# Performance work log

Measured on AMD Instinct MI355X. Metric: run time of the kernel, lower is better.

Reference implementation:

```python
import jax, jax.numpy as jnp
import numpy as np

L = 8192            # sequence length
V = 100000          # vocab size
E = 256             # embedding dim
H = 512             # lstm hidden dim (bidirectional total)
HD = H // 2         # per-direction hidden
TAGS = 32
T = TAGS + 2        # tagset + START/STOP
START = T - 2       # START_TAG = -2
STOP = T - 1        # STOP_TAG = -1
NEG = -10000.0


def setup_inputs() -> dict:
    key = jax.random.key(0)
    ks = jax.random.split(key, 11)
    s = 0.05
    return {
        "input_words": jax.random.randint(ks[0], (L,), 0, V),
        "embed": jax.random.normal(ks[1], (V, E), dtype=jnp.float32) * s,
        "Wih_f": jax.random.normal(ks[2], (4 * HD, E), dtype=jnp.float32) * s,
        "Whh_f": jax.random.normal(ks[3], (4 * HD, HD), dtype=jnp.float32) * s,
        "b_f": jax.random.normal(ks[4], (4 * HD,), dtype=jnp.float32) * s,
        "Wih_b": jax.random.normal(ks[5], (4 * HD, E), dtype=jnp.float32) * s,
        "Whh_b": jax.random.normal(ks[6], (4 * HD, HD), dtype=jnp.float32) * s,
        "b_b": jax.random.normal(ks[7], (4 * HD,), dtype=jnp.float32) * s,
        "W_out": jax.random.normal(ks[8], (T, H), dtype=jnp.float32) * s,
        "b_out": jax.random.normal(ks[9], (T,), dtype=jnp.float32) * s,
        "transitions": jax.random.normal(ks[10], (T, T), dtype=jnp.float32),
    }


def _lstm_dir(x, Wih, Whh, b, reverse):
    # single-layer LSTM, one direction; torch gate order i, f, g, o
    def step(carry, xt):
        h, c = carry
        g = xt @ Wih.T + h @ Whh.T + b
        i, f, gg, o = jnp.split(g, 4)
        i = jax.nn.sigmoid(i)
        f = jax.nn.sigmoid(f)
        gg = jnp.tanh(gg)
        o = jax.nn.sigmoid(o)
        c = f * c + i * gg
        h = o * jnp.tanh(c)
        return (h, c), h

    init = (jnp.zeros((HD,), x.dtype), jnp.zeros((HD,), x.dtype))
    _, hs = jax.lax.scan(step, init, x, reverse=reverse)
    return hs  # (L, HD)


def _crf_marginals(feats, transitions):
    lse = jax.nn.logsumexp
    # forward algorithm: alpha_t[j] = lse_i(alpha_{t-1}[i] + trans[j,i]) + feat_t[j]
    def fstep(alpha, feat):
        new = lse(alpha[None, :] + transitions, axis=1) + feat
        return new, new

    alpha0 = jnp.full((T,), NEG, feats.dtype).at[START].set(0.0)
    alphaL, log_alpha = jax.lax.scan(fstep, alpha0, feats)  # (L, T)

    # backward algorithm, replicating repo's init: beta_L[j] = lse_i(trans[i, j])
    beta_last = lse(transitions, axis=0)

    # beta_t[j] = lse_i(beta_{t+1}[i] + feat_{t+1}[i] + trans[i, j])
    def bstep(beta, feat_next):
        new = lse((beta + feat_next)[:, None] + transitions, axis=0)
        return new, new

    _, betas = jax.lax.scan(bstep, beta_last, feats[1:], reverse=True)
    log_beta = jnp.concatenate([betas, beta_last[None]], axis=0)  # (L, T)
    return log_alpha + log_beta


def reference(input_words, embed, Wih_f, Whh_f, b_f, Wih_b, Whh_b, b_b,
              W_out, b_out, transitions):
    x = embed[input_words]                           # (L, E)
    hf = _lstm_dir(x, Wih_f, Whh_f, b_f, reverse=False)
    hb = _lstm_dir(x, Wih_b, Whh_b, b_b, reverse=True)
    lstm_out = jnp.concatenate([hf, hb], axis=-1)    # (L, H)
    feats = lstm_out @ W_out.T + b_out               # (L, T)
    score = _crf_marginals(feats, transitions)       # (L, T)
    tags = jnp.argmax(score, axis=1)                 # (L,)
    return score, tags
```

## Files before the change

### kernel.cpp

```cpp
#include <hip/hip_runtime.h>
#include <cstdint>
#include <cstddef>

#define LSEQ 8192
#define NT   34
#define NP   36
#define SCH  64
#define CCH  128
#define F_L2E 1.4426950408889634f
#define F_LN2 0.6931471805599453f

typedef int v4i __attribute__((ext_vector_type(4)));

#if __has_builtin(__builtin_amdgcn_global_load_lds)
#define HAS_GLL 1
#else
#define HAS_GLL 0
#endif

#if __has_builtin(__builtin_amdgcn_mfma_i32_16x16x64_i8)
#define MFMA_I8(a,b,c) __builtin_amdgcn_mfma_i32_16x16x64_i8((a),(b),(c),0,0,0)
#else
__device__ __forceinline__ v4i mfma_i8_asm(v4i a, v4i b, v4i c){
  asm volatile("v_mfma_i32_16x16x64_i8 %0, %1, %2, %0\n\ts_nop 7\n\ts_nop 7"
               : "+v"(c) : "v"(a), "v"(b));
  return c;
}
#define MFMA_I8(a,b,c) mfma_i8_asm((a),(b),(c))
#endif

__device__ __forceinline__ float ex2(float x){
#if __has_builtin(__builtin_amdgcn_exp2f)
  return __builtin_amdgcn_exp2f(x);
#else
  return exp2f(x);
#endif
}
__device__ __forceinline__ float lg2(float x){
#if __has_builtin(__builtin_amdgcn_logf)
  return __builtin_amdgcn_logf(x);
#else
  return __log2f(x);
#endif
}

__device__ __forceinline__ float sigf(float x){
  return __fdividef(1.f, 1.f + ex2(-F_L2E * x));
}
__device__ __forceinline__ float tanhf_fast(float x){
  return 1.f - __fdividef(2.f, ex2(2.f * F_L2E * x) + 1.f);
}

__device__ __forceinline__ void barrier_lds(){
  asm volatile("s_waitcnt lgkmcnt(0)\n\ts_barrier" ::: "memory");
}

__global__ void k_quant(const float* __restrict__ Whh_f,
                        const float* __restrict__ Whh_b,
                        int* __restrict__ Wq, float* __restrict__ fac){
  int bid = blockIdx.x;
  int dir = bid >> 10;
  int r   = bid & 1023;
  int i   = threadIdx.x;
  const float* W = (dir ? Whh_b : Whh_f) + r * 256 + i * 4;
  float w0 = W[0], w1 = W[1], w2 = W[2], w3 = W[3];
  float m = fmaxf(fmaxf(fabsf(w0), fabsf(w1)), fmaxf(fabsf(w2), fabsf(w3)));
  for (int s = 32; s; s >>= 1) m = fmaxf(m, __shfl_xor(m, s));
  float scale = (m > 0.f) ? m / 127.f : 1.f;
  float inv = __fdividef(1.f, scale);
  int q0 = (int)rintf(w0 * inv), q1 = (int)rintf(w1 * inv);
  int q2 = (int)rintf(w2 * inv), q3 = (int)rintf(w3 * inv);
  q0 = max(-127, min(127, q0)); q1 = max(-127, min(127, q1));
  q2 = max(-127, min(127, q2)); q3 = max(-127, min(127, q3));
  int p = (q0 & 255) | ((q1 & 255) << 8) | ((q2 & 255) << 16) | ((q3 & 255) << 24);
  Wq[(dir << 16) + (r << 6) + i] = p;
  if (i == 0) fac[(dir << 10) + r] = scale * (1.f / 127.f);
}

__global__ void k_gproj(const int* __restrict__ words,
                        const float* __restrict__ embed,
                        const float* __restrict__ Wih_f, const float* __restrict__ b_f,
                        const float* __restrict__ Wih_b, const float* __restrict__ b_b,
                        float* __restrict__ G_f, float* __restrict__ G_b){
  int dir = blockIdx.y;
  const float* Wih = dir ? Wih_b : Wih_f;
  const float* bb  = dir ? b_b  : b_f;
  float* G = dir ? G_b : G_f;
  int t0 = blockIdx.x * 16;
  __shared__ __align__(16) float X[16 * 256];
  for (int idx = threadIdx.x; idx < 16 * 256; idx += 256) {
    int tt = idx >> 8, e = idx & 255;
    X[idx] = embed[(size_t)words[t0 + tt] * 256 + e];
  }
  __syncthreads();
  const float4* X4 = (const float4*)X;
  for (int rb = 0; rb < 4; rb++) {
    int r = rb * 256 + threadIdx.x;
    float bv = bb[r];
    float acc[16];
#pragma unroll
    for (int tt = 0; tt < 16; tt++) acc[tt] = bv;
    const float4* W4 = (const float4*)(Wih + (size_t)r * 256);
    for (int eb = 0; eb < 64; eb++) {
      float4 w = W4[eb];
#pragma unroll
      for (int tt = 0; tt < 16; tt++) {
        float4 x = X4[tt * 64 + eb];
        acc[tt] += w.x * x.x + w.y * x.y + w.z * x.z + w.w * x.w;
      }
    }
    for (int tt = 0; tt < 16; tt++)
      G[(size_t)(t0 + tt) * 1024 + (threadIdx.x << 2) + rb] = acc[tt];
  }
}

__global__ __launch_bounds__(512, 2) void k_lstm(const int* __restrict__ Wq,
                                                 const float* __restrict__ fac,
                                                 const float* __restrict__ G_f,
                                                 const float* __restrict__ G_b,
                                                 float* __restrict__ hf,
                                                 float* __restrict__ hb){
  int dir = blockIdx.x;
  const int* Wqd = Wq + (dir << 16);
  const float* facp = fac + (dir << 10);
  const float* G = dir ? G_b : G_f;
  float* hout = dir ? hb : hf;
  int tid = threadIdx.x;
  int ln  = tid & 63;
  int wv  = tid >> 6;
  int lg  = ln >> 4;
  int lr  = ln & 15;
  int h_l = (lr >> 2) & 1;
  int r_l = lr & 3;
  int u   = (wv << 5) + (h_l << 4) + (lg << 2) + r_l;

  __shared__ __align__(16) float GL[2][4 * 1024];
  __shared__ __align__(16) int h8c[2][64];

  v4i wgt[4][2][4];
#pragma unroll
  for (int g = 0; g < 4; g++)
#pragma unroll
    for (int h = 0; h < 2; h++) {
      int R = g * 256 + (wv << 5) + (h << 4) + lr;
#pragma unroll
      for (int ks = 0; ks < 4; ks++)
        wgt[g][h][ks] = *(const v4i*)(Wqd + R * 64 + ks * 16 + lg * 4);
    }

  float fI = facp[u], fF = facp[u + 256], fG = facp[u + 512], fO = facp[u + 768];
  if (tid < 64) h8c[0][tid] = 0;
  float c = 0.f;
  v4i zero = {0, 0, 0, 0};

  auto stage = [&](int cn) {
    int half = cn & 1;
    int gt0 = dir ? (8191 - (cn * 4 + 3)) : (cn * 4);
    const char* src = (const char*)(G + (size_t)gt0 * 1024) + (wv << 11) + (ln << 4);
    char* dst = (char*)&GL[half][0] + (wv << 11);
#pragma unroll
    for (int i = 0; i < 2; i++) {
#if HAS_GLL
      __builtin_amdgcn_global_load_lds(
          (const __attribute__((address_space(1))) unsigned int*)(src + (i << 10)),
          (__attribute__((address_space(3))) unsigned int*)(dst + (i << 10)),
          16, 0, 0);
#else
      *(float4*)(dst + (i << 10) + (ln << 4)) = *(const float4*)(src + (i << 10));
#endif
    }
  };

  auto step = [&](int t, const float* Grow, const int* bufR, int* bufW) {
    const v4i* hb4 = (const v4i*)bufR;
    v4i b0 = hb4[lg], b1 = hb4[4 + lg], b2 = hb4[8 + lg], b3 = hb4[12 + lg];
    float4 gv = ((const float4*)Grow)[u];
    v4i res[4][2];
#pragma unroll
    for (int g = 0; g < 4; g++)
#pragma unroll
      for (int h = 0; h < 2; h++)
        res[g][h] = MFMA_I8(wgt[g][h][0], b0, zero);
#pragma unroll
    for (int g = 0; g < 4; g++)
#pragma unroll
      for (int h = 0; h < 2; h++)
        res[g][h] = MFMA_I8(wgt[g][h][1], b1, res[g][h]);
#pragma unroll
    for (int g = 0; g < 4; g++)
#pragma unroll
      for (int h = 0; h < 2; h++)
        res[g][h] = MFMA_I8(wgt[g][h][2], b2, res[g][h]);
#pragma unroll
    for (int g = 0; g < 4; g++)
#pragma unroll
      for (int h = 0; h < 2; h++)
        res[g][h] = MFMA_I8(wgt[g][h][3], b3, res[g][h]);
    bool sh = h_l != 0;
    bool s1 = (r_l & 1) != 0;
    bool s2 = (r_l & 2) != 0;
    v4i tI = sh ? res[0][1] : res[0][0];
    v4i tF = sh ? res[1][1] : res[1][0];
    v4i tG = sh ? res[2][1] : res[2][0];
    v4i tO = sh ? res[3][1] : res[3][0];
    int vI = s2 ? (s1 ? tI.w : tI.z) : (s1 ? tI.y : tI.x);
    int vF = s2 ? (s1 ? tF.w : tF.z) : (s1 ? tF.y : tF.x);
    int vG = s2 ? (s1 ? tG.w : tG.z) : (s1 ? tG.y : tG.x);
    int vO = s2 ? (s1 ? tO.w : tO.z) : (s1 ? tO.y : tO.x);
    float ri = (float)vI * fI + gv.x;
    float rf = (float)vF * fF + gv.y;
    float rg = (float)vG * fG + gv.z;
    float ro = (float)vO * fO + gv.w;
    float is = sigf(ri), fs = sigf(rf);
    float gt = tanhf_fast(rg), os = sigf(ro);
    c = fs * c + is * gt;
    float hv = os * tanhf_fast(c);
    int q = ((int)rintf(hv * 127.f)) & 255;
    int x = q << (r_l * 8);
#if __has_builtin(__builtin_amdgcn_mov_dpp)
    x += __builtin_amdgcn_mov_dpp(x, 0xB1, 0xF, 0xF, true);
    x += __builtin_amdgcn_mov_dpp(x, 0x4E, 0xF, 0xF, true);
#else
    x += __shfl_xor(x, 1);
    x += __shfl_xor(x, 2);
#endif
    if (r_l == 0 && lr < 8) bufW[u >> 2] = x;
    if (lr < 8) {
      int time = dir ? (8191 - t) : t;
      hout[(size_t)time * 256 + u] = hv;
    }
  };

  stage(0);
  asm volatile("s_waitcnt vmcnt(0)" ::: "memory");
  __syncthreads();

  int cur = 0;
  for (int cn = 0; cn < 2048; ++cn) {
    if (cn + 1 < 2048) stage(cn + 1);
    const float* Hc = GL[cn & 1];
#pragma unroll
    for (int s = 0; s < 4; ++s) {
      int row = dir ? (3 - s) : s;
      step((cn << 2) + s, Hc + (row << 10), h8c[cur], h8c[cur ^ 1]);
      cur ^= 1;
      if (s == 3) {
        asm volatile("s_waitcnt vmcnt(0) lgkmcnt(0)\n\ts_barrier" ::: "memory");
      } else {
        barrier_lds();
      }
    }
  }
}

__global__ void k_feats(const float* __restrict__ hf, const float* __restrict__ hb,
                        const float* __restrict__ W_out, const float* __restrict__ b_out,
                        float* __restrict__ feats){
  int t0 = blockIdx.x * 16;
  for (int oi = threadIdx.x; oi < 16 * NT; oi += 256) {
    int tt = oi / NT;
    int tag = oi - tt * NT;
    int t = t0 + tt;
    const float4* w4 = (const float4*)(W_out + (size_t)tag * 512);
    const float4* a4 = (const float4*)(hf + (size_t)t * 256);
    const float4* c4 = (const float4*)(hb + (size_t)t * 256);
    float acc = b_out[tag];
    for (int k = 0; k < 64; k++) {
      float4 w = w4[k]; float4 h = a4[k];
      acc += w.x * h.x + w.y * h.y + w.z * h.z + w.w * h.w;
    }
    for (int k = 0; k < 64; k++) {
      float4 w = w4[64 + k]; float4 h = c4[k];
      acc += w.x * h.x + w.y * h.y + w.z * h.z + w.w * h.w;
    }
    feats[(size_t)t * NT + tag] = acc;
  }
}

__global__ __launch_bounds__(320) void k_crf_p1(const float* __restrict__ feats,
                                                const float* __restrict__ trans,
                                                float* __restrict__ Pg,
                                                float* __restrict__ rmaxG){
  int dir = blockIdx.x >> 7;
  int c   = blockIdx.x & (CCH - 1);
  int tid = threadIdx.x;
  int t0  = c * SCH;

  __shared__ __align__(16) float TRM[NT * NP];
  __shared__ float Fe[(SCH + 1) * NT];
  __shared__ __align__(16) float Pbuf[2][NT * NP];
  __shared__ float CM[NP];
  __shared__ float RMs[NT];

  for (int idx = tid; idx < NT * NT; idx += 320) {
    int j = idx / NT, k = idx - j * NT;
    float v = (dir == 0) ? trans[j * NT + k] : trans[k * NT + j];
    TRM[j * NP + k] = v * F_L2E;
  }
  for (int idx = tid; idx < (SCH + 1) * NT; idx += 320) {
    int s = idx / NT, j = idx - s * NT;
    int t = t0 + s; if (t > LSEQ - 1) t = LSEQ - 1;
    Fe[idx] = feats[(size_t)t * NT + j] * F_L2E;
  }
  for (int idx = tid; idx < NT * NP; idx += 320) {
    int k = idx / NP, i = idx - k * NP;
    Pbuf[0][idx] = (i < NT && i == k) ? 0.f : -1e30f;
  }
  if (tid < NP) CM[tid] = (tid < NT) ? 0.f : -1e30f;
  __syncthreads();
  if (tid < NT) {
    float m = -3e38f;
    for (int k = 0; k < NT; k++) m = fmaxf(m, TRM[tid * NP + k]);
    RMs[tid] = m;
  }
  __syncthreads();
  for (int idx = tid; idx < NT * NT; idx += 320) {
    int j = idx / NT, k = idx - j * NT;
    TRM[j * NP + k] -= RMs[j];
  }
  __syncthreads();

  int cur = 0;
  int j = tid / 9, g = tid - (tid / 9) * 9;
  bool act = (tid < 306);
  int i0 = 4 * g;

  for (int s = 0; s < SCH; s++) {
    int t = (dir == 0) ? (t0 + s) : (t0 + SCH - 1 - s);
    if (dir == 1 && t == LSEQ - 1) continue;
    const float* Pc = Pbuf[cur];
    float* Pn = Pbuf[cur ^ 1];
    if (act) {
      float cm0 = CM[i0], cm1 = CM[i0 + 1], cm2 = CM[i0 + 2], cm3 = CM[i0 + 3];
      float s0 = 0, s1 = 0, s2 = 0, s3 = 0;
      const float* trp = TRM + j * NP;
      const float* fep = Fe + (t + 1 - t0) * NT;
#pragma unroll
      for (int k = 0; k < NT; k++) {
        float trv = trp[k];
        if (dir == 1) trv += fep[k];
        float4 p = *(const float4*)&Pc[k * NP + i0];
        s0 += ex2(trv + p.x - cm0);
        s1 += ex2(trv + p.y - cm1);
        s2 += ex2(trv + p.z - cm2);
        s3 += ex2(trv + p.w - cm3);
      }
      float base = RMs[j] + ((dir == 0) ? Fe[(t - t0) * NT + j] : 0.f);
      float4 o;
      o.x = base + cm0 + lg2(s0);
      o.y = base + cm1 + lg2(s1);
      o.z = (i0 + 2 < NT) ? (base + cm2 + lg2(s2)) : -1e30f;
      o.w = (i0 + 3 < NT) ? (base + cm3 + lg2(s3)) : -1e30f;
      *(float4*)&Pn[j * NP + i0] = o;
    }
    __syncthreads();
    if (tid < NP) {
      float m = -3e38f;
      const float* col = Pn + tid;
      for (int k = 0; k < NT; k++) m = fmaxf(m, col[k * NP]);
      CM[tid] = m;
    }
    cur ^= 1;
    __syncthreads();
  }

  const float* Pf = Pbuf[cur];
  size_t base = (size_t)((dir << 7) + c) * (NT * NP);
  for (int idx = tid; idx < NT * NP; idx += 320)
    Pg[base + idx] = Pf[idx];
  if (tid < NT) {
    float m = -3e38f;
    for (int i = 0; i < NT; i++) m = fmaxf(m, Pf[tid * NP + i]);
    rmaxG[((dir << 7) + c) * NT + tid] = m;
  }
}

__global__ void k_crf_p2(const float* __restrict__ trans,
                         const float* __restrict__ Pg,
                         const float* __restrict__ rmaxG,
                         float* __restrict__ vIn){
  int dir = blockIdx.x;
  int lane = threadIdx.x;
  bool a = (lane < NT);
  int j = a ? lane : 0;
  __shared__ float V[NP];

  float v;
  if (dir == 0) {
    v = (lane == 32) ? 0.f : -10000.f * F_L2E;
  } else {
    float m = -3e38f;
    for (int i = 0; i < NT; i++) m = fmaxf(m, trans[i * NT + j]);
    float s = 0.f;
    for (int i = 0; i < NT; i++) s += ex2((trans[i * NT + j] - m) * F_L2E);
    v = m * F_L2E + lg2(s);
  }
  if (lane < NP) V[lane] = -1e30f;
  barrier_lds();
  if (a) V[j] = v;
  barrier_lds();
  float vm = a ? v : -3e38f;
  for (int off = 32; off; off >>= 1) vm = fmaxf(vm, __shfl_xor(vm, off));

  if (a) {
    int c0 = (dir == 0) ? 0 : (CCH - 1);
    vIn[((size_t)(dir << 7) + c0) * NP + j] = v;
  }

  for (int it = 0; it < CCH - 1; it++) {
    int c = (dir == 0) ? it : (CCH - 1 - it);
    const float* row = Pg + ((size_t)(dir << 7) + c) * (NT * NP) + j * NP;
    float rm = rmaxG[((dir << 7) + c) * NT + j];
    float m = rm + vm;
    float s = 0.f;
#pragma unroll
    for (int k = 0; k < NP; k += 4) {
      float4 p = *(const float4*)&row[k];
      s += ex2(p.x + V[k]     - m);
      s += ex2(p.y + V[k + 1] - m);
      s += ex2(p.z + V[k + 2] - m);
      s += ex2(p.w + V[k + 3] - m);
    }
    float nv = m + lg2(s);
    if (a) V[j] = nv;
    barrier_lds();
    float x = a ? nv : -3e38f;
    for (int off = 32; off; off >>= 1) x = fmaxf(x, __shfl_xor(x, off));
    vm = x;
    int cn = (dir == 0) ? (c + 1) : (c - 1);
    if (a) vIn[((size_t)(dir << 7) + cn) * NP + j] = nv;
  }
}

__global__ void k_crf_p3(const float* __restrict__ feats,
                         const float* __restrict__ trans,
                         const float* __restrict__ vIn,
                         float* __restrict__ wsA,
                         float* __restrict__ wsB){
  int dir = blockIdx.x >> 7;
  int c   = blockIdx.x & (CCH - 1);
  int lane = threadIdx.x;
  int t0 = c * SCH;
  bool a = (lane < NT);
  int j = a ? lane : 0;
  __shared__ float A[NP];
  __shared__ float U[NP];

  float trr[NT];
  float rm = -3e38f;
#pragma unroll
  for (int k = 0; k < NT; k++) {
    float vv = (dir == 0) ? trans[j * NT + k] : trans[k * NT + j];
    trr[k] = vv * F_L2E;
    rm = fmaxf(rm, trr[k]);
  }
  if (lane < NP) { A[lane] = -1e30f; U[lane] = -1e30f; }
  float v0 = vIn[((size_t)(dir << 7) + c) * NP + j];
  barrier_lds();
  if (a) A[j] = v0;
  barrier_lds();
  float am = a ? v0 : -3e38f;
  for (int off = 32; off; off >>= 1) am = fmaxf(am, __shfl_xor(am, off));

  if (dir == 0) {
    float fe = feats[(size_t)t0 * NT + j] * F_L2E;
    for (int s = 0; s < SCH; s++) {
      int t = t0 + s;
      int tn = (t + 1 < LSEQ) ? t + 1 : LSEQ - 1;
      float fe_n = feats[(size_t)tn * NT + j] * F_L2E;
      float m = rm + am;
      float ss = 0.f;
#pragma unroll
      for (int k = 0; k < NT; k++) ss += ex2(trr[k] + A[k] - m);
      float out = m + lg2(ss) + fe;
      if (a) wsA[(size_t)t * NT + j] = out * F_LN2;
      if (a) A[j] = out;
      barrier_lds();
      float x = a ? out : -3e38f;
      for (int off = 32; off; off >>= 1) x = fmaxf(x, __shfl_xor(x, off));
      am = x;
      fe = fe_n;
    }
  } else {
    float b = v0;
    int tfirst = t0 + SCH; if (tfirst > LSEQ - 1) tfirst = LSEQ - 1;
    float fe = feats[(size_t)tfirst * NT + j] * F_L2E;
    for (int s = 0; s < SCH; s++) {
      int t = t0 + SCH - 1 - s;
      float fe_n = feats[(size_t)t * NT + j] * F_L2E;
      float out;
      if (t == LSEQ - 1) {
        out = b;
      } else {
        if (a) U[j] = b + fe;
        barrier_lds();
        float um = a ? U[j] : -3e38f;
        for (int off = 32; off; off >>= 1) um = fmaxf(um, __shfl_xor(um, off));
        float m = rm + um;
        float ss = 0.f;
#pragma unroll
        for (int k = 0; k < NT; k++) ss += ex2(trr[k] + U[k] - m);
        out = m + lg2(ss);
        barrier_lds();
      }
      if (a) wsB[(size_t)t * NT + j] = out * F_LN2;
      b = out;
      fe = fe_n;
    }
  }
}

__global__ void k_finish(const float* __restrict__ wsA, const float* __restrict__ wsB,
                         float* __restrict__ out){
  int t = blockIdx.x * 256 + threadIdx.x;
  float m = -3e38f; int bi = 0;
  for (int i = 0; i < NT; i++) {
    float sc = wsA[(size_t)t * NT + i] + wsB[(size_t)t * NT + i];
    out[(size_t)t * NT + i] = sc;
    if (sc > m) { m = sc; bi = i; }
  }
  out[(size_t)LSEQ * NT + t] = (float)bi;
}

extern "C" void kernel_launch(void* const* d_in, const int* in_sizes, int n_in,
                              void* d_out, int out_size, void* d_ws, size_t ws_size,
                              hipStream_t stream) {
  const int*   words  = (const int*)  d_in[0];
  const float* embed  = (const float*)d_in[1];
  const float* Wih_f  = (const float*)d_in[2];
  const float* Whh_f  = (const float*)d_in[3];
  const float* b_f    = (const float*)d_in[4];
  const float* Wih_b  = (const float*)d_in[5];
  const float* Whh_b  = (const float*)d_in[6];
  const float* b_b    = (const float*)d_in[7];
  const float* W_out  = (const float*)d_in[8];
  const float* b_out  = (const float*)d_in[9];
  const float* trans  = (const float*)d_in[10];
  float* out = (float*)d_out;

  float* wsf = (float*)d_ws;
  size_t off = 0;
  float* G_f   = wsf + off; off += (size_t)LSEQ * 1024;
  float* G_b   = wsf + off; off += (size_t)LSEQ * 1024;
  float* hf    = wsf + off; off += (size_t)LSEQ * 256;
  float* hb    = wsf + off; off += (size_t)LSEQ * 256;
  float* feats = wsf + off; off += (size_t)LSEQ * NT + 16;
  float* wsA   = wsf + off; off += (size_t)LSEQ * NT + 16;
  float* wsB   = wsf + off; off += (size_t)LSEQ * NT + 16;
  float* fac   = wsf + off; off += 2048;
  int*   Wq    = (int*)(wsf + off); off += 2 * 1024 * 64;
  float* Pg    = G_f;
  float* rmaxG = G_f + 256 * (NT * NP);
  float* vIn   = rmaxG + 256 * NT + 32;

  k_quant<<<2048, 64, 0, stream>>>(Whh_f, Whh_b, Wq, fac);
  k_gproj<<<dim3(512, 2), 256, 0, stream>>>(words, embed, Wih_f, b_f, Wih_b, b_b, G_f, G_b);
  k_lstm<<<2, 512, 0, stream>>>(Wq, fac, G_f, G_b, hf, hb);
  k_feats<<<512, 256, 0, stream>>>(hf, hb, W_out, b_out, feats);
  k_crf_p1<<<256, 320, 0, stream>>>(feats, trans, Pg, rmaxG);
  k_crf_p2<<<2, 64, 0, stream>>>(trans, Pg, rmaxG, vIn);
  k_crf_p3<<<256, 64, 0, stream>>>(feats, trans, vIn, wsA, wsB);
  k_finish<<<32, 256, 0, stream>>>(wsA, wsB, out);
}
```

Before: 8.128 ms.

## Split LSTM recurrence units between MFMA waves and sdot4 VALU waves

The 8 waves of the LSTM recurrence block are split into two roles. Waves 0-3 keep computing hidden units 0-127 with int8 MFMA. Waves 4-7 compute units 128-255 with VALU sdot4 dot products and a 4-lane DPP reduction, and write their int8 hidden bytes straight to LDS. The goal is to shorten the per-step serial MFMA chain by running matrix-core and vector work side by side. The cost is higher VALU instruction counts and register pressure, plus possible imbalance between the two roles at each step.

After: 10.43 ms. 1.28x slower.

```diff
diff --git a/kernel.cpp b/kernel.cpp
--- a/kernel.cpp
+++ b/kernel.cpp
@@ -18,6 +18,19 @@
 #define HAS_GLL 0
 #endif
 
+#if __has_builtin(__builtin_amdgcn_sdot4)
+#define DOT4(a,b,c) __builtin_amdgcn_sdot4((a),(b),(c),false)
+#else
+__device__ __forceinline__ int dot4_fb(int a,int b,int c){
+  c += (int)(signed char)(a & 0xff)        * (int)(signed char)(b & 0xff);
+  c += (int)(signed char)((a>>8) & 0xff)   * (int)(signed char)((b>>8) & 0xff);
+  c += (int)(signed char)((a>>16) & 0xff)  * (int)(signed char)((b>>16) & 0xff);
+  c += (a>>24) * (b>>24);
+  return c;
+}
+#define DOT4(a,b,c) dot4_fb((a),(b),(c))
+#endif
+
 #if __has_builtin(__builtin_amdgcn_mfma_i32_16x16x64_i8)
 #define MFMA_I8(a,b,c) __builtin_amdgcn_mfma_i32_16x16x64_i8((a),(b),(c),0,0,0)
 #else
@@ -49,6 +62,17 @@
 }
 __device__ __forceinline__ float tanhf_fast(float x){
   return 1.f - __fdividef(2.f, ex2(2.f * F_L2E * x) + 1.f);
+}
+
+__device__ __forceinline__ int qreduce(int x){
+#if __has_builtin(__builtin_amdgcn_mov_dpp)
+  x += __builtin_amdgcn_mov_dpp(x, 0xB1, 0xF, 0xF, true);
+  x += __builtin_amdgcn_mov_dpp(x, 0x4E, 0xF, 0xF, true);
+#else
+  x += __shfl_xor(x, 1);
+  x += __shfl_xor(x, 2);
+#endif
+  return x;
 }
 
 __device__ __forceinline__ void barrier_lds(){
@@ -128,25 +152,41 @@
   int tid = threadIdx.x;
   int ln  = tid & 63;
   int wv  = tid >> 6;
+  bool mrole = (wv < 4);
+
   int lg  = ln >> 4;
   int lr  = ln & 15;
   int h_l = (lr >> 2) & 1;
   int r_l = lr & 3;
-  int u   = (wv << 5) + (h_l << 4) + (lg << 2) + r_l;
+  int kq  = ln & 3;
+  int ub  = 128 + ((wv & 3) << 5) + ((ln >> 2) << 1);
+
+  int u = mrole ? ((wv << 5) + (h_l << 4) + (lg << 2) + r_l)
+                : (ub + (ln & 1));
 
   __shared__ __align__(16) float GL[2][4 * 1024];
   __shared__ __align__(16) int h8c[2][64];
 
-  v4i wgt[4][2][4];
-#pragma unroll
-  for (int g = 0; g < 4; g++)
-#pragma unroll
-    for (int h = 0; h < 2; h++) {
-      int R = g * 256 + (wv << 5) + (h << 4) + lr;
-#pragma unroll
-      for (int ks = 0; ks < 4; ks++)
-        wgt[g][h][ks] = *(const v4i*)(Wqd + R * 64 + ks * 16 + lg * 4);
-    }
+  v4i wgt[32];
+  if (mrole) {
+#pragma unroll
+    for (int g = 0; g < 4; g++)
+#pragma unroll
+      for (int h = 0; h < 2; h++) {
+        int R = g * 256 + (wv << 5) + (h << 4) + lr;
+#pragma unroll
+        for (int ks = 0; ks < 4; ks++)
+          wgt[(g * 2 + h) * 4 + ks] = *(const v4i*)(Wqd + R * 64 + ks * 16 + lg * 4);
+      }
+  } else {
+#pragma unroll
+    for (int m = 0; m < 8; m++) {
+      int R = (m >> 1) * 256 + ub + (m & 1);
+      const v4i* p = (const v4i*)(Wqd + R * 64 + kq * 16);
+#pragma unroll
+      for (int j = 0; j < 4; j++) wgt[m * 4 + j] = p[j];
+    }
+  }
 
   float fI = facp[u], fF = facp[u + 256], fG = facp[u + 512], fO = facp[u + 768];
   if (tid < 64) h8c[0][tid] = 0;
@@ -172,41 +212,70 @@
   };
 
   auto step = [&](int t, const float* Grow, const int* bufR, int* bufW) {
-    const v4i* hb4 = (const v4i*)bufR;
-    v4i b0 = hb4[lg], b1 = hb4[4 + lg], b2 = hb4[8 + lg], b3 = hb4[12 + lg];
     float4 gv = ((const float4*)Grow)[u];
-    v4i res[4][2];
-#pragma unroll
-    for (int g = 0; g < 4; g++)
-#pragma unroll
-      for (int h = 0; h < 2; h++)
-        res[g][h] = MFMA_I8(wgt[g][h][0], b0, zero);
-#pragma unroll
-    for (int g = 0; g < 4; g++)
-#pragma unroll
-      for (int h = 0; h < 2; h++)
-        res[g][h] = MFMA_I8(wgt[g][h][1], b1, res[g][h]);
-#pragma unroll
-    for (int g = 0; g < 4; g++)
-#pragma unroll
-      for (int h = 0; h < 2; h++)
-        res[g][h] = MFMA_I8(wgt[g][h][2], b2, res[g][h]);
-#pragma unroll
-    for (int g = 0; g < 4; g++)
-#pragma unroll
-      for (int h = 0; h < 2; h++)
-        res[g][h] = MFMA_I8(wgt[g][h][3], b3, res[g][h]);
-    bool sh = h_l != 0;
-    bool s1 = (r_l & 1) != 0;
-    bool s2 = (r_l & 2) != 0;
-    v4i tI = sh ? res[0][1] : res[0][0];
-    v4i tF = sh ? res[1][1] : res[1][0];
-    v4i tG = sh ? res[2][1] : res[2][0];
-    v4i tO = sh ? res[3][1] : res[3][0];
-    int vI = s2 ? (s1 ? tI.w : tI.z) : (s1 ? tI.y : tI.x);
-    int vF = s2 ? (s1 ? tF.w : tF.z) : (s1 ? tF.y : tF.x);
-    int vG = s2 ? (s1 ? tG.w : tG.z) : (s1 ? tG.y : tG.x);
-    int vO = s2 ? (s1 ? tO.w : tO.z) : (s1 ? tO.y : tO.x);
+    int vI, vF, vG, vO;
+    if (mrole) {
+      const v4i* hb4 = (const v4i*)bufR;
+      v4i b0 = hb4[lg], b1 = hb4[4 + lg], b2 = hb4[8 + lg], b3 = hb4[12 + lg];
+      v4i res[4][2];
+#pragma unroll
+      for (int g = 0; g < 4; g++)
+#pragma unroll
+        for (int h = 0; h < 2; h++)
+          res[g][h] = MFMA_I8(wgt[(g * 2 + h) * 4 + 0], b0, zero);
+#pragma unroll
+      for (int g = 0; g < 4; g++)
+#pragma unroll
+        for (int h = 0; h < 2; h++)
+          res[g][h] = MFMA_I8(wgt[(g * 2 + h) * 4 + 1], b1, res[g][h]);
+#pragma unroll
+      for (int g = 0; g < 4; g++)
+#pragma unroll
+        for (int h = 0; h < 2; h++)
+          res[g][h] = MFMA_I8(wgt[(g * 2 + h) * 4 + 2], b2, res[g][h]);
+#pragma unroll
+      for (int g = 0; g < 4; g++)
+#pragma unroll
+        for (int h = 0; h < 2; h++)
+          res[g][h] = MFMA_I8(wgt[(g * 2 + h) * 4 + 3], b3, res[g][h]);
+      bool sh = h_l != 0;
+      bool s1 = (r_l & 1) != 0;
+      bool s2 = (r_l & 2) != 0;
+      v4i tI = sh ? res[0][1] : res[0][0];
+      v4i tF = sh ? res[1][1] : res[1][0];
+      v4i tG = sh ? res[2][1] : res[2][0];
+      v4i tO = sh ? res[3][1] : res[3][0];
+      vI = s2 ? (s1 ? tI.w : tI.z) : (s1 ? tI.y : tI.x);
+      vF = s2 ? (s1 ? tF.w : tF.z) : (s1 ? tF.y : tF.x);
+      vG = s2 ? (s1 ? tG.w : tG.z) : (s1 ? tG.y : tG.x);
+      vO = s2 ? (s1 ? tO.w : tO.z) : (s1 ? tO.y : tO.x);
+    } else {
+      const v4i* hs = (const v4i*)((const char*)bufR + (kq << 6));
+      v4i h0 = hs[0], h1 = hs[1], h2 = hs[2], h3 = hs[3];
+      int acc[8];
+#pragma unroll
+      for (int m = 0; m < 8; m++) {
+        int a = 0;
+        v4i w0 = wgt[m * 4 + 0], w1 = wgt[m * 4 + 1];
+        v4i w2 = wgt[m * 4 + 2], w3 = wgt[m * 4 + 3];
+        a = DOT4(w0.x, h0.x, a); a = DOT4(w0.y, h0.y, a);
+        a = DOT4(w0.z, h0.z, a); a = DOT4(w0.w, h0.w, a);
+        a = DOT4(w1.x, h1.x, a); a = DOT4(w1.y, h1.y, a);
+        a = DOT4(w1.z, h1.z, a); a = DOT4(w1.w, h1.w, a);
+        a = DOT4(w2.x, h2.x, a); a = DOT4(w2.y, h2.y, a);
+        a = DOT4(w2.z, h2.z, a); a = DOT4(w2.w, h2.w, a);
+        a = DOT4(w3.x, h3.x, a); a = DOT4(w3.y, h3.y, a);
+        a = DOT4(w3.z, h3.z, a); a = DOT4(w3.w, h3.w, a);
+        acc[m] = a;
+      }
+#pragma unroll
+      for (int m = 0; m < 8; m++) acc[m] = qreduce(acc[m]);
+      int p_ = ln & 1;
+      vI = p_ ? acc[1] : acc[0];
+      vF = p_ ? acc[3] : acc[2];
+      vG = p_ ? acc[5] : acc[4];
+      vO = p_ ? acc[7] : acc[6];
+    }
     float ri = (float)vI * fI + gv.x;
     float rf = (float)vF * fF + gv.y;
     float rg = (float)vG * fG + gv.z;
@@ -215,19 +284,24 @@
     float gt = tanhf_fast(rg), os = sigf(ro);
     c = fs * c + is * gt;
     float hv = os * tanhf_fast(c);
-    int q = ((int)rintf(hv * 127.f)) & 255;
-    int x = q << (r_l * 8);
+    int time = dir ? (8191 - t) : t;
+    if (mrole) {
+      int q = ((int)rintf(hv * 127.f)) & 255;
+      int x = q << (r_l * 8);
 #if __has_builtin(__builtin_amdgcn_mov_dpp)
-    x += __builtin_amdgcn_mov_dpp(x, 0xB1, 0xF, 0xF, true);
-    x += __builtin_amdgcn_mov_dpp(x, 0x4E, 0xF, 0xF, true);
-#else
-    x += __shfl_xor(x, 1);
-    x += __shfl_xor(x, 2);
-#endif
-    if (r_l == 0 && lr < 8) bufW[u >> 2] = x;
-    if (lr < 8) {
-      int time = dir ? (8191 - t) : t;
-      hout[(size_t)time * 256 + u] = hv;
+      x += __builtin_amdgcn_mov_dpp(x, 0xB1, 0xF, 0xF, true);
+      x += __builtin_amdgcn_mov_dpp(x, 0x4E, 0xF, 0xF, true);
+#else
+      x += __shfl_xor(x, 1);
+      x += __shfl_xor(x, 2);
+#endif
+      if (r_l == 0 && lr < 8) bufW[u >> 2] = x;
+      if (lr < 8) hout[(size_t)time * 256 + u] = hv;
+    } else {
+      if ((ln & 3) < 2) {
+        ((signed char*)bufW)[u] = (signed char)(int)rintf(hv * 127.f);
+        hout[(size_t)time * 256 + u] = hv;
+      }
     }
   };
 
```
